# Performance work log

Measured on AMD Instinct MI355X. Metric: run time of the kernel, lower is better.

## Reference

```python
import jax, jax.numpy as jnp
import numpy as np


def setup_inputs() -> dict:
    key = jax.random.key(0)
    ks = jax.random.split(key, 6)
    b, t, s, qu, vu, d = 8, 64, 512, 512, 512, 512
    return {
        "query": jax.random.normal(ks[0], (b, t, qu), jnp.float32),
        "value": jax.random.normal(ks[1], (b, s, vu), jnp.float32),
        "mask": jax.random.randint(ks[2], (b, s), 0, 2).astype(bool),
        "W1_w": jax.random.normal(ks[3], (qu, d), jnp.float32) * (1.0 / np.sqrt(qu)),
        "W1_b": jnp.zeros((d,), jnp.float32),
        "W2_w": jax.random.normal(ks[4], (vu, d), jnp.float32) * (1.0 / np.sqrt(vu)),
        "W2_b": jnp.zeros((d,), jnp.float32),
        "scale": jax.random.normal(ks[5], (d,), jnp.float32) * 0.05,
    }


def reference(query, value, mask, W1_w, W1_b, W2_w, W2_b, scale):
    # Dense projections
    q = jnp.einsum('btq,qd->btd', query, W1_w) + W1_b   # [b,t,d]
    k = jnp.einsum('bsv,vd->bsd', value, W2_w) + W2_b   # [b,s,d]
    # Additive (Bahdanau) score with learned scale vector (Keras use_scale=True)
    # scores[b,t,s] = sum_d scale[d] * tanh(q[b,t,d] + k[b,s,d])
    scores = jnp.einsum('btsd,d->bts', jnp.tanh(q[:, :, None, :] + k[:, None, :, :]), scale)
    # Mask over source positions (value mask); query mask is all-ones (no-op)
    scores = jnp.where(mask[:, None, :], scores, jnp.float32(-1e9))
    attention_weights = jax.nn.softmax(scores, axis=-1)   # [b,t,s]
    context_vector = jnp.einsum('bts,bsv->btv', attention_weights, value)  # [b,t,vu]
    return context_vector, attention_weights
```

## Files before the change

kernel.cpp:

```cpp
#include <hip/hip_runtime.h>
#include <hip/hip_bf16.h>

#define B_  8
#define T_  64
#define S_  512
#define D_  512

#define QN (512 * 512)
#define KN (4096 * 512)

#define TLOG2E 2.8853900817779268f
#define LOG2E  1.4426950408889634f

typedef __attribute__((ext_vector_type(8))) short bf16x8;
typedef __attribute__((ext_vector_type(4))) float f32x4;

__device__ __forceinline__ unsigned int pk2(float a, float b) {
    float2 f; f.x = a; f.y = b;
    __hip_bfloat162 h = __float22bfloat162_rn(f);
    return *(unsigned int*)&h;
}

__global__ __launch_bounds__(256) void mfma_gemm(
    const float* __restrict__ query, const float* __restrict__ value,
    const float* __restrict__ W1, const float* __restrict__ W2,
    const float* __restrict__ b1, const float* __restrict__ b2,
    float* __restrict__ qproj, float* __restrict__ kproj)
{
    __shared__ __align__(16) unsigned short Ab[2][64][40];
    __shared__ __align__(16) unsigned short Bs[2][64][40];

    const int x = blockIdx.x;
    const float *A, *W;
    float* C;
    int tm, tn;
    bool isq;
    if (x < 512) {
        tm = (x & 7) * 8 + ((x >> 3) & 7);
        tn = x >> 6;
        A = value; W = W2; C = kproj; isq = false;
    } else {
        int r = x - 512;
        tm = r >> 3; tn = r & 7;
        A = query; W = W1; C = qproj; isq = true;
    }

    const int tid  = threadIdx.x;
    const int lane = tid & 63;
    const int wid  = tid >> 6;
    const int wm = (wid & 1) * 32, wn = (wid >> 1) * 32;
    const int fm = lane & 15, fq = lane >> 4;

    f32x4 acc00 = {0.f, 0.f, 0.f, 0.f};
    f32x4 acc01 = acc00, acc10 = acc00, acc11 = acc00;

    const int ar = tid >> 2;
    const int ac = (tid & 3) * 8;
    const float* Ag = A + (size_t)(tm * 64 + ar) * 512 + ac;
    const int c0 = (tid & 15) * 4;
    const int kp = (tid >> 4) * 2;
    const float* Wg = W + (size_t)kp * 512 + tn * 64 + c0;

    float4 av0, av1, wv0, wv1;

#define STAGE(BUF) do {                                                       \
        uint4 pa;                                                             \
        pa.x = pk2(av0.x, av0.y); pa.y = pk2(av0.z, av0.w);                   \
        pa.z = pk2(av1.x, av1.y); pa.w = pk2(av1.z, av1.w);                   \
        *(uint4*)&Ab[BUF][ar][ac] = pa;                                       \
        *(unsigned int*)&Bs[BUF][c0 + 0][kp] = pk2(wv0.x, wv1.x);             \
        *(unsigned int*)&Bs[BUF][c0 + 1][kp] = pk2(wv0.y, wv1.y);             \
        *(unsigned int*)&Bs[BUF][c0 + 2][kp] = pk2(wv0.z, wv1.z);             \
        *(unsigned int*)&Bs[BUF][c0 + 3][kp] = pk2(wv0.w, wv1.w);             \
    } while (0)

    av0 = *(const float4*)(Ag);
    av1 = *(const float4*)(Ag + 4);
    wv0 = *(const float4*)(Wg);
    wv1 = *(const float4*)(Wg + 512);
    STAGE(0);
    av0 = *(const float4*)(Ag + 32);
    av1 = *(const float4*)(Ag + 36);
    wv0 = *(const float4*)(Wg + 32 * 512);
    wv1 = *(const float4*)(Wg + 33 * 512);
    __syncthreads();

#pragma unroll
    for (int i = 0; i < 16; ++i) {
        const int cur = i & 1, nxt = cur ^ 1;
        bf16x8 a0  = *(const bf16x8*)&Ab[cur][wm + fm][fq * 8];
        bf16x8 a1  = *(const bf16x8*)&Ab[cur][wm + 16 + fm][fq * 8];
        bf16x8 b0  = *(const bf16x8*)&Bs[cur][wn + fm][fq * 8];
        bf16x8 b1v = *(const bf16x8*)&Bs[cur][wn + 16 + fm][fq * 8];
        if (i < 15) {
            STAGE(nxt);
            const int kn = ((i + 2) & 15) * 32;
            av0 = *(const float4*)(Ag + kn);
            av1 = *(const float4*)(Ag + kn + 4);
            wv0 = *(const float4*)(Wg + (size_t)kn * 512);
            wv1 = *(const float4*)(Wg + (size_t)kn * 512 + 512);
        }
        acc00 = __builtin_amdgcn_mfma_f32_16x16x32_bf16(a0, b0,  acc00, 0, 0, 0);
        acc01 = __builtin_amdgcn_mfma_f32_16x16x32_bf16(a0, b1v, acc01, 0, 0, 0);
        acc10 = __builtin_amdgcn_mfma_f32_16x16x32_bf16(a1, b0,  acc10, 0, 0, 0);
        acc11 = __builtin_amdgcn_mfma_f32_16x16x32_bf16(a1, b1v, acc11, 0, 0, 0);
        __syncthreads();
    }
#undef STAGE

    const int n0 = tn * 64 + wn + fm;
    const int n1 = n0 + 16;
    float bias0 = 0.f, bias1 = 0.f;
    if (isq) {
        bias0 = b1[n0] + b2[n0];
        bias1 = b1[n1] + b2[n1];
    }
    const int m0 = tm * 64 + wm + fq * 4;
#pragma unroll
    for (int r = 0; r < 4; ++r) {
        C[(size_t)(m0 + r) * 512 + n0]      = (acc00[r] + bias0) * TLOG2E;
        C[(size_t)(m0 + r) * 512 + n1]      = (acc01[r] + bias1) * TLOG2E;
        C[(size_t)(m0 + 16 + r) * 512 + n0] = (acc10[r] + bias0) * TLOG2E;
        C[(size_t)(m0 + 16 + r) * 512 + n1] = (acc11[r] + bias1) * TLOG2E;
    }
}

__global__ __launch_bounds__(1024) void fused_attn(
    const float* __restrict__ qproj, const float* __restrict__ kproj,
    const int*   __restrict__ mask,  const float* __restrict__ scale,
    const float* __restrict__ value,
    float* __restrict__ ctx, float* __restrict__ attn)
{
    const int blk = blockIdx.x;
    const int b  = blk & 7;
    const int tp = blk >> 3;
    const size_t row0 = (size_t)(b * T_ + tp * 2);

    __shared__ __align__(16) float q0A[512];
    __shared__ __align__(16) float dA[512];
    __shared__ __align__(16) float cA[512];
    __shared__ __align__(16) float2 pex[512];
    __shared__ __align__(16) float2 wp2[512];
    __shared__ __align__(16) float4 part[2][8][128];
    __shared__ float2 red2[16];

    const int tid  = threadIdx.x;
    const int lane = tid & 63;
    const int wid  = tid >> 6;

    if (tid < 512) {
        float q0v = qproj[row0 * D_ + tid];
        float q1v = qproj[(row0 + 1) * D_ + tid];
        q0A[tid] = q0v;
        dA[tid]  = __builtin_amdgcn_exp2f(q1v - q0v);
        cA[tid]  = scale[tid];
    }
    __syncthreads();

    const int s    = tid & 511;
    const int half = tid >> 9;
    const int dlo  = half << 8;
    const int m = mask[b * S_ + s];
    const float* kr = kproj + (size_t)(b * S_ + s) * D_ + dlo;
    float p0 = 0.f, p1 = 0.f;

    float4 kf0 = ((const float4*)kr)[0];
    float4 kf1 = ((const float4*)kr)[1];
    float4 kf2 = ((const float4*)kr)[2];
    float4 kf3 = ((const float4*)kr)[3];

#define SC_STEP(K4, DD) do {                                                  \
        float4 q4 = *(const float4*)&q0A[DD];                                 \
        float4 dl = *(const float4*)&dA[DD];                                  \
        float4 c4 = *(const float4*)&cA[DD];                                  \
        float e, ra, rb;                                                      \
        e  = __builtin_amdgcn_exp2f(q4.x + (K4).x);                           \
        ra = __builtin_amdgcn_rcpf(e + 1.0f);                                 \
        rb = __builtin_amdgcn_rcpf(fmaf(e, dl.x, 1.0f));                      \
        p0 = fmaf(c4.x, ra, p0); p1 = fmaf(c4.x, rb, p1);                     \
        e  = __builtin_amdgcn_exp2f(q4.y + (K4).y);                           \
        ra = __builtin_amdgcn_rcpf(e + 1.0f);                                 \
        rb = __builtin_amdgcn_rcpf(fmaf(e, dl.y, 1.0f));                      \
        p0 = fmaf(c4.y, ra, p0); p1 = fmaf(c4.y, rb, p1);                     \
        e  = __builtin_amdgcn_exp2f(q4.z + (K4).z);                           \
        ra = __builtin_amdgcn_rcpf(e + 1.0f);                                 \
        rb = __builtin_amdgcn_rcpf(fmaf(e, dl.z, 1.0f));                      \
        p0 = fmaf(c4.z, ra, p0); p1 = fmaf(c4.z, rb, p1);                     \
        e  = __builtin_amdgcn_exp2f(q4.w + (K4).w);                           \
        ra = __builtin_amdgcn_rcpf(e + 1.0f);                                 \
        rb = __builtin_amdgcn_rcpf(fmaf(e, dl.w, 1.0f));                      \
        p0 = fmaf(c4.w, ra, p0); p1 = fmaf(c4.w, rb, p1);                     \
    } while (0)

    for (int c = 0; c < 16; ++c) {
        const int nx = ((c + 1) & 15) * 16;
        float4 nf0 = ((const float4*)(kr + nx))[0];
        float4 nf1 = ((const float4*)(kr + nx))[1];
        float4 nf2 = ((const float4*)(kr + nx))[2];
        float4 nf3 = ((const float4*)(kr + nx))[3];
        const int d0 = dlo + c * 16;
        SC_STEP(kf0, d0);
        SC_STEP(kf1, d0 + 4);
        SC_STEP(kf2, d0 + 8);
        SC_STEP(kf3, d0 + 12);
        kf0 = nf0; kf1 = nf1; kf2 = nf2; kf3 = nf3;
    }
#undef SC_STEP

    if (half == 1) { float2 pp; pp.x = p0; pp.y = p1; pex[s] = pp; }
    __syncthreads();

    float x0 = 0.f, x1 = 0.f;
    if (tid < 512) {
        float2 ph = pex[s];
        p0 += ph.x; p1 += ph.y;
        x0 = m ? (-2.0f * p0) : -1e9f;
        x1 = m ? (-2.0f * p1) : -1e9f;
        float2 mx; mx.x = x0; mx.y = x1;
#pragma unroll
        for (int off = 32; off >= 1; off >>= 1) {
            mx.x = fmaxf(mx.x, __shfl_xor(mx.x, off));
            mx.y = fmaxf(mx.y, __shfl_xor(mx.y, off));
        }
        if (lane == 0) red2[wid] = mx;
    }
    __syncthreads();

    float e0 = 0.f, e1 = 0.f;
    if (tid < 512) {
        float2 M = red2[0];
#pragma unroll
        for (int i = 1; i < 8; ++i) {
            M.x = fmaxf(M.x, red2[i].x);
            M.y = fmaxf(M.y, red2[i].y);
        }
        e0 = __builtin_amdgcn_exp2f((x0 - M.x) * LOG2E);
        e1 = __builtin_amdgcn_exp2f((x1 - M.y) * LOG2E);
        float2 sm; sm.x = e0; sm.y = e1;
#pragma unroll
        for (int off = 32; off >= 1; off >>= 1) {
            sm.x += __shfl_xor(sm.x, off);
            sm.y += __shfl_xor(sm.y, off);
        }
        if (lane == 0) red2[8 + wid] = sm;
    }
    __syncthreads();

    if (tid < 512) {
        float2 SS = red2[8];
#pragma unroll
        for (int i = 9; i < 16; ++i) {
            SS.x += red2[i].x;
            SS.y += red2[i].y;
        }
        const float w0 = e0 * __builtin_amdgcn_rcpf(SS.x);
        const float w1 = e1 * __builtin_amdgcn_rcpf(SS.y);
        float2 wpair; wpair.x = w0; wpair.y = w1;
        wp2[s] = wpair;
        attn[row0 * S_ + s]       = w0;
        attn[(row0 + 1) * S_ + s] = w1;
    }
    __syncthreads();

    const int g  = tid >> 7;
    const int v4 = tid & 127;
    const float* vb = value + ((size_t)(b * S_) + g * 64) * D_ + v4 * 4;
    float4 a0; a0.x = 0.f; a0.y = 0.f; a0.z = 0.f; a0.w = 0.f;
    float4 a1 = a0;
#pragma unroll 4
    for (int i = 0; i < 64; ++i) {
        float4 vv = *(const float4*)(vb + (size_t)i * D_);
        float2 w = wp2[g * 64 + i];
        a0.x = fmaf(w.x, vv.x, a0.x); a0.y = fmaf(w.x, vv.y, a0.y);
        a0.z = fmaf(w.x, vv.z, a0.z); a0.w = fmaf(w.x, vv.w, a0.w);
        a1.x = fmaf(w.y, vv.x, a1.x); a1.y = fmaf(w.y, vv.y, a1.y);
        a1.z = fmaf(w.y, vv.z, a1.z); a1.w = fmaf(w.y, vv.w, a1.w);
    }
    part[0][g][v4] = a0;
    part[1][g][v4] = a1;
    __syncthreads();
    if (tid < 256) {
        const int t = tid >> 7, v = tid & 127;
        float4 o; o.x = 0.f; o.y = 0.f; o.z = 0.f; o.w = 0.f;
#pragma unroll
        for (int gg = 0; gg < 8; ++gg) {
            float4 p = part[t][gg][v];
            o.x += p.x; o.y += p.y; o.z += p.z; o.w += p.w;
        }
        *(float4*)(ctx + (row0 + t) * D_ + v * 4) = o;
    }
}

extern "C" void kernel_launch(void* const* d_in, const int* in_sizes, int n_in,
                              void* d_out, int out_size, void* d_ws, size_t ws_size,
                              hipStream_t stream) {
    const float* query = (const float*)d_in[0];
    const float* value = (const float*)d_in[1];
    const int*   mask  = (const int*)  d_in[2];
    const float* W1w   = (const float*)d_in[3];
    const float* W1b   = (const float*)d_in[4];
    const float* W2w   = (const float*)d_in[5];
    const float* W2b   = (const float*)d_in[6];
    const float* scale = (const float*)d_in[7];

    float* ctx  = (float*)d_out;
    float* attn = (float*)d_out + (size_t)B_ * T_ * D_;

    float* qproj = (float*)d_ws;
    float* kproj = qproj + (size_t)QN;

    mfma_gemm<<<576, 256, 0, stream>>>(query, value, W1w, W2w, W1b, W2b,
                                       qproj, kproj);
    fused_attn<<<256, 1024, 0, stream>>>(qproj, kproj, mask, scale, value,
                                         ctx, attn);
}
```

Baseline: 133.8 us.

## Store key projection transposed and split score loop over d-quarters

The GEMM epilogue now writes the key projection transposed per batch ([b][d][s]) with float4 stores. The score kernel has each thread handle two adjacent source positions over a quarter of d, so a wavefront's key loads become coalesced float2 reads along s instead of each thread striding through its own row. Partial sums from the four d-quarters are combined through shared memory. This gives up the per-thread float4 row loads and adds a four-way reduction and more q/scale shared-memory reads per element.

```diff
diff --git a/kernel.cpp b/kernel.cpp
--- a/kernel.cpp
+++ b/kernel.cpp
@@ -25,7 +25,7 @@
     const float* __restrict__ query, const float* __restrict__ value,
     const float* __restrict__ W1, const float* __restrict__ W2,
     const float* __restrict__ b1, const float* __restrict__ b2,
-    float* __restrict__ qproj, float* __restrict__ kproj)
+    float* __restrict__ qproj, float* __restrict__ kT)
 {
     __shared__ __align__(16) unsigned short Ab[2][64][40];
     __shared__ __align__(16) unsigned short Bs[2][64][40];
@@ -38,7 +38,7 @@
     if (x < 512) {
         tm = (x & 7) * 8 + ((x >> 3) & 7);
         tn = x >> 6;
-        A = value; W = W2; C = kproj; isq = false;
+        A = value; W = W2; C = kT; isq = false;
     } else {
         int r = x - 512;
         tm = r >> 3; tn = r & 7;
@@ -110,23 +110,39 @@
 
     const int n0 = tn * 64 + wn + fm;
     const int n1 = n0 + 16;
-    float bias0 = 0.f, bias1 = 0.f;
+    const int m0 = tm * 64 + wm + fq * 4;
     if (isq) {
-        bias0 = b1[n0] + b2[n0];
-        bias1 = b1[n1] + b2[n1];
-    }
-    const int m0 = tm * 64 + wm + fq * 4;
-#pragma unroll
-    for (int r = 0; r < 4; ++r) {
-        C[(size_t)(m0 + r) * 512 + n0]      = (acc00[r] + bias0) * TLOG2E;
-        C[(size_t)(m0 + r) * 512 + n1]      = (acc01[r] + bias1) * TLOG2E;
-        C[(size_t)(m0 + 16 + r) * 512 + n0] = (acc10[r] + bias0) * TLOG2E;
-        C[(size_t)(m0 + 16 + r) * 512 + n1] = (acc11[r] + bias1) * TLOG2E;
+        float bias0 = b1[n0] + b2[n0];
+        float bias1 = b1[n1] + b2[n1];
+#pragma unroll
+        for (int r = 0; r < 4; ++r) {
+            C[(size_t)(m0 + r) * 512 + n0]      = (acc00[r] + bias0) * TLOG2E;
+            C[(size_t)(m0 + r) * 512 + n1]      = (acc01[r] + bias1) * TLOG2E;
+            C[(size_t)(m0 + 16 + r) * 512 + n0] = (acc10[r] + bias0) * TLOG2E;
+            C[(size_t)(m0 + 16 + r) * 512 + n1] = (acc11[r] + bias1) * TLOG2E;
+        }
+    } else {
+        const int bb = m0 >> 9;
+        const int sl = m0 & 511;
+        float* kb = C + (size_t)(bb * 512) * 512;
+        float4 o;
+        o.x = acc00[0] * TLOG2E; o.y = acc00[1] * TLOG2E;
+        o.z = acc00[2] * TLOG2E; o.w = acc00[3] * TLOG2E;
+        *(float4*)(kb + (size_t)n0 * 512 + sl) = o;
+        o.x = acc10[0] * TLOG2E; o.y = acc10[1] * TLOG2E;
+        o.z = acc10[2] * TLOG2E; o.w = acc10[3] * TLOG2E;
+        *(float4*)(kb + (size_t)n0 * 512 + sl + 16) = o;
+        o.x = acc01[0] * TLOG2E; o.y = acc01[1] * TLOG2E;
+        o.z = acc01[2] * TLOG2E; o.w = acc01[3] * TLOG2E;
+        *(float4*)(kb + (size_t)n1 * 512 + sl) = o;
+        o.x = acc11[0] * TLOG2E; o.y = acc11[1] * TLOG2E;
+        o.z = acc11[2] * TLOG2E; o.w = acc11[3] * TLOG2E;
+        *(float4*)(kb + (size_t)n1 * 512 + sl + 16) = o;
     }
 }
 
 __global__ __launch_bounds__(1024) void fused_attn(
-    const float* __restrict__ qproj, const float* __restrict__ kproj,
+    const float* __restrict__ qproj, const float* __restrict__ kT,
     const int*   __restrict__ mask,  const float* __restrict__ scale,
     const float* __restrict__ value,
     float* __restrict__ ctx, float* __restrict__ attn)
@@ -139,7 +155,7 @@
     __shared__ __align__(16) float q0A[512];
     __shared__ __align__(16) float dA[512];
     __shared__ __align__(16) float cA[512];
-    __shared__ __align__(16) float2 pex[512];
+    __shared__ __align__(16) float4 pex[4][256];
     __shared__ __align__(16) float2 wp2[512];
     __shared__ __align__(16) float4 part[2][8][128];
     __shared__ float2 red2[16];
@@ -157,65 +173,67 @@
     }
     __syncthreads();
 
-    const int s    = tid & 511;
-    const int half = tid >> 9;
-    const int dlo  = half << 8;
-    const int m = mask[b * S_ + s];
-    const float* kr = kproj + (size_t)(b * S_ + s) * D_ + dlo;
-    float p0 = 0.f, p1 = 0.f;
-
-    float4 kf0 = ((const float4*)kr)[0];
-    float4 kf1 = ((const float4*)kr)[1];
-    float4 kf2 = ((const float4*)kr)[2];
-    float4 kf3 = ((const float4*)kr)[3];
-
-#define SC_STEP(K4, DD) do {                                                  \
-        float4 q4 = *(const float4*)&q0A[DD];                                 \
-        float4 dl = *(const float4*)&dA[DD];                                  \
-        float4 c4 = *(const float4*)&cA[DD];                                  \
-        float e, ra, rb;                                                      \
-        e  = __builtin_amdgcn_exp2f(q4.x + (K4).x);                           \
-        ra = __builtin_amdgcn_rcpf(e + 1.0f);                                 \
-        rb = __builtin_amdgcn_rcpf(fmaf(e, dl.x, 1.0f));                      \
-        p0 = fmaf(c4.x, ra, p0); p1 = fmaf(c4.x, rb, p1);                     \
-        e  = __builtin_amdgcn_exp2f(q4.y + (K4).y);                           \
-        ra = __builtin_amdgcn_rcpf(e + 1.0f);                                 \
-        rb = __builtin_amdgcn_rcpf(fmaf(e, dl.y, 1.0f));                      \
-        p0 = fmaf(c4.y, ra, p0); p1 = fmaf(c4.y, rb, p1);                     \
-        e  = __builtin_amdgcn_exp2f(q4.z + (K4).z);                           \
-        ra = __builtin_amdgcn_rcpf(e + 1.0f);                                 \
-        rb = __builtin_amdgcn_rcpf(fmaf(e, dl.z, 1.0f));                      \
-        p0 = fmaf(c4.z, ra, p0); p1 = fmaf(c4.z, rb, p1);                     \
-        e  = __builtin_amdgcn_exp2f(q4.w + (K4).w);                           \
-        ra = __builtin_amdgcn_rcpf(e + 1.0f);                                 \
-        rb = __builtin_amdgcn_rcpf(fmaf(e, dl.w, 1.0f));                      \
-        p0 = fmaf(c4.w, ra, p0); p1 = fmaf(c4.w, rb, p1);                     \
+    const int sp  = tid & 255;
+    const int dq  = tid >> 8;
+    const int dlo = dq * 128;
+    const float* kb = kT + ((size_t)(b * 512 + dlo)) * 512 + sp * 2;
+
+    float p00 = 0.f, p10 = 0.f, p01 = 0.f, p11 = 0.f;
+
+    float2 nf0 = *(const float2*)(kb);
+    float2 nf1 = *(const float2*)(kb + 512);
+    float2 nf2 = *(const float2*)(kb + 1024);
+    float2 nf3 = *(const float2*)(kb + 1536);
+
+#define SC2(KF, QV, DV, CV) do {                                              \
+        float e0 = __builtin_amdgcn_exp2f((QV) + (KF).x);                     \
+        float ra = __builtin_amdgcn_rcpf(e0 + 1.0f);                          \
+        float rb = __builtin_amdgcn_rcpf(fmaf(e0, (DV), 1.0f));               \
+        p00 = fmaf((CV), ra, p00); p10 = fmaf((CV), rb, p10);                 \
+        float e1 = __builtin_amdgcn_exp2f((QV) + (KF).y);                     \
+        float rc = __builtin_amdgcn_rcpf(e1 + 1.0f);                          \
+        float rd = __builtin_amdgcn_rcpf(fmaf(e1, (DV), 1.0f));               \
+        p01 = fmaf((CV), rc, p01); p11 = fmaf((CV), rd, p11);                 \
     } while (0)
 
-    for (int c = 0; c < 16; ++c) {
-        const int nx = ((c + 1) & 15) * 16;
-        float4 nf0 = ((const float4*)(kr + nx))[0];
-        float4 nf1 = ((const float4*)(kr + nx))[1];
-        float4 nf2 = ((const float4*)(kr + nx))[2];
-        float4 nf3 = ((const float4*)(kr + nx))[3];
-        const int d0 = dlo + c * 16;
-        SC_STEP(kf0, d0);
-        SC_STEP(kf1, d0 + 4);
-        SC_STEP(kf2, d0 + 8);
-        SC_STEP(kf3, d0 + 12);
-        kf0 = nf0; kf1 = nf1; kf2 = nf2; kf3 = nf3;
-    }
-#undef SC_STEP
-
-    if (half == 1) { float2 pp; pp.x = p0; pp.y = p1; pex[s] = pp; }
+    for (int g = 0; g < 32; ++g) {
+        float2 kf0 = nf0, kf1 = nf1, kf2 = nf2, kf3 = nf3;
+        const float* nb = kb + (size_t)(((g + 1) & 31) * 4) * 512;
+        nf0 = *(const float2*)(nb);
+        nf1 = *(const float2*)(nb + 512);
+        nf2 = *(const float2*)(nb + 1024);
+        nf3 = *(const float2*)(nb + 1536);
+        const int d0 = dlo + g * 4;
+        float4 q4 = *(const float4*)&q0A[d0];
+        float4 dl = *(const float4*)&dA[d0];
+        float4 c4 = *(const float4*)&cA[d0];
+        SC2(kf0, q4.x, dl.x, c4.x);
+        SC2(kf1, q4.y, dl.y, c4.y);
+        SC2(kf2, q4.z, dl.z, c4.z);
+        SC2(kf3, q4.w, dl.w, c4.w);
+    }
+#undef SC2
+
+    {
+        float4 pq; pq.x = p00; pq.y = p10; pq.z = p01; pq.w = p11;
+        pex[dq][sp] = pq;
+    }
     __syncthreads();
 
     float x0 = 0.f, x1 = 0.f;
     if (tid < 512) {
-        float2 ph = pex[s];
-        p0 += ph.x; p1 += ph.y;
-        x0 = m ? (-2.0f * p0) : -1e9f;
-        x1 = m ? (-2.0f * p1) : -1e9f;
+        const int s = tid;
+        const int s2 = s >> 1;
+        const bool odd = (s & 1) != 0;
+        float4 r0 = pex[0][s2], r1 = pex[1][s2];
+        float4 r2 = pex[2][s2], r3 = pex[3][s2];
+        float pt0 = odd ? ((r0.z + r1.z) + (r2.z + r3.z))
+                        : ((r0.x + r1.x) + (r2.x + r3.x));
+        float pt1 = odd ? ((r0.w + r1.w) + (r2.w + r3.w))
+                        : ((r0.y + r1.y) + (r2.y + r3.y));
+        const int m = mask[b * S_ + s];
+        x0 = m ? (-2.0f * pt0) : -1e9f;
+        x1 = m ? (-2.0f * pt1) : -1e9f;
         float2 mx; mx.x = x0; mx.y = x1;
 #pragma unroll
         for (int off = 32; off >= 1; off >>= 1) {
@@ -247,6 +265,7 @@
     __syncthreads();
 
     if (tid < 512) {
+        const int s = tid;
         float2 SS = red2[8];
 #pragma unroll
         for (int i = 9; i < 16; ++i) {
@@ -307,10 +326,10 @@
     float* attn = (float*)d_out + (size_t)B_ * T_ * D_;
 
     float* qproj = (float*)d_ws;
-    float* kproj = qproj + (size_t)QN;
+    float* kT    = qproj + (size_t)QN;
 
     mfma_gemm<<<576, 256, 0, stream>>>(query, value, W1w, W2w, W1b, W2b,
-                                       qproj, kproj);
-    fused_attn<<<256, 1024, 0, stream>>>(qproj, kproj, mask, scale, value,
+                                       qproj, kT);
+    fused_attn<<<256, 1024, 0, stream>>>(qproj, kT, mask, scale, value,
                                          ctx, attn);
 }
```

Measured after the change: 126.5 us. 1.06x faster.
